# Kernel optimization log

Measured on AMD Instinct MI355X. Metric: run time of the kernel, lower is better.

The kernel has to match this reference:

```python
import jax, jax.numpy as jnp
import numpy as np

DIM = 256
HEADS = 8
HEAD_DIM = DIM // HEADS


def setup_inputs() -> dict:
    key = jax.random.key(0)
    ks = jax.random.split(key, 10)
    B, Nq, Nk, C = 2, 2048, 2048, DIM
    inp = {
        "query": jax.random.normal(ks[0], (B, Nq, C), jnp.float32),
        "key": jax.random.normal(ks[1], (B, Nk, C), jnp.float32),
        "value": jax.random.normal(ks[2], (B, Nk, C), jnp.float32),
        "qpos": jnp.zeros((B, Nq), jnp.int32),
        "kpos": jnp.zeros((B, Nk), jnp.int32),
        "mask": jax.random.randint(ks[3], (Nq, Nk), 0, 2) > 0,
        "similarities": jax.random.normal(ks[4], (B, HEADS, Nq, Nk), jnp.float32),
        # learned params (torch Linear stored here as [C_in, C_out]; no qkv bias)
        "Wq": jax.random.normal(ks[5], (C, C), jnp.float32) / np.sqrt(C),
        "Wk": jax.random.normal(ks[6], (C, C), jnp.float32) / np.sqrt(C),
        "Wv": jax.random.normal(ks[7], (C, C), jnp.float32) / np.sqrt(C),
        "Wp": jax.random.normal(ks[8], (C, C), jnp.float32) / np.sqrt(C),
        "bp": jax.random.normal(ks[9], (C,), jnp.float32) * 0.01,
    }
    return inp


def reference(query, key, value, qpos, kpos, mask, similarities, Wq, Wk, Wv, Wp, bp):
    B, Nq, C = query.shape
    Nk = key.shape[1]
    H, hd = HEADS, HEAD_DIM
    scale = hd ** -0.5
    # projections -> [B, N, H, hd] (rope is None, so qpos/kpos are unused)
    q = (query @ Wq).reshape(B, Nq, H, hd)
    k = (key @ Wk).reshape(B, Nk, H, hd)
    v = (value @ Wv).reshape(B, Nk, H, hd)
    # scores [B, H, Nq, Nk]
    attn = jnp.einsum("bqhd,bkhd->bhqk", q, k) * scale
    # mean-centered similarity bias (mean over heads, dim=1)
    attn = attn + (similarities - similarities.mean(axis=1, keepdims=True))
    # boolean mask: fill False positions with -inf, then softmax over keys
    attn = jnp.where(mask[None, None, :, :], attn, -jnp.inf)
    attn = jax.nn.softmax(attn, axis=-1)
    # AV -> [B, Nq, C], output projection
    x = jnp.einsum("bhqk,bkhd->bqhd", attn, v).reshape(B, Nq, C)
    return x @ Wp + bp
```

## Files before the change

### kernel.cpp

```cpp
#include <hip/hip_runtime.h>

#define B_  2
#define NQ  2048
#define NK  2048
#define C_  256
#define H_  8
#define HD  32

typedef float f32x4 __attribute__((ext_vector_type(4)));
typedef __bf16 bf16x8 __attribute__((ext_vector_type(8)));
typedef unsigned short ushort8 __attribute__((ext_vector_type(8)));

static __device__ __forceinline__ unsigned short f2bf(float f) {
    unsigned int u = __builtin_bit_cast(unsigned int, f);
    u += 0x7FFFu + ((u >> 16) & 1u);
    return (unsigned short)(u >> 16);
}
static __device__ __forceinline__ float bf2f(unsigned short h) {
    unsigned int u = ((unsigned int)h) << 16;
    return __builtin_bit_cast(float, u);
}
static __device__ __forceinline__ unsigned int split1(float f) {
    unsigned short h = f2bf(f);
    unsigned short l = f2bf(f - bf2f(h));
    return (unsigned int)h | ((unsigned int)l << 16);
}
static __device__ __forceinline__ bf16x8 ld_bf16x8(const unsigned short* p) {
    return __builtin_bit_cast(bf16x8, *(const ushort8*)p);
}
static __device__ __forceinline__ void async16(const void* g, void* l) {
    __builtin_amdgcn_global_load_lds((__attribute__((address_space(1))) void*)g,
                                     (__attribute__((address_space(3))) void*)l,
                                     16, 0, 0);
}

__global__ __launch_bounds__(256) void proj_kernel(const float* __restrict__ X,
                                                   const float* __restrict__ W,
                                                   unsigned short* __restrict__ dh,
                                                   unsigned short* __restrict__ dl,
                                                   int vmode)
{
    __shared__ unsigned short WtH[64][32];
    __shared__ unsigned short WtL[64][32];

    const int tid  = threadIdx.x;
    const int wave = tid >> 6;
    const int lane = tid & 63;
    const int n15  = lane & 15;
    const int quad = lane >> 4;
    const int m0   = blockIdx.x * 64;
    const int j0   = blockIdx.y * 64;

    f32x4 acc[4];
    acc[0] = 0.f; acc[1] = 0.f; acc[2] = 0.f; acc[3] = 0.f;

    const int sj  = tid >> 2;
    const int skc = (tid & 3) * 8;
    const float* __restrict__ xrow = X + (size_t)(m0 + wave * 16 + n15) * C_;

    for (int k0 = 0; k0 < C_; k0 += 32) {
        ushort8 wh, wl;
        #pragma unroll
        for (int i = 0; i < 8; ++i) {
            unsigned int p = split1(W[(size_t)(k0 + skc + i) * C_ + j0 + sj]);
            wh[i] = (unsigned short)p;
            wl[i] = (unsigned short)(p >> 16);
        }
        *(ushort8*)&WtH[sj][skc] = wh;
        *(ushort8*)&WtL[sj][skc] = wl;
        __syncthreads();

        f32x4 a0 = *(const f32x4*)(xrow + k0 + quad * 8);
        f32x4 a1 = *(const f32x4*)(xrow + k0 + quad * 8 + 4);
        ushort8 ah, al;
        #pragma unroll
        for (int i = 0; i < 4; ++i) {
            unsigned int p0 = split1(a0[i]);
            unsigned int p1 = split1(a1[i]);
            ah[i]     = (unsigned short)p0;  al[i]     = (unsigned short)(p0 >> 16);
            ah[i + 4] = (unsigned short)p1;  al[i + 4] = (unsigned short)(p1 >> 16);
        }
        bf16x8 Ah = __builtin_bit_cast(bf16x8, ah);
        bf16x8 Al = __builtin_bit_cast(bf16x8, al);

        #pragma unroll
        for (int f = 0; f < 4; ++f) {
            bf16x8 Bh = ld_bf16x8(&WtH[f * 16 + n15][quad * 8]);
            bf16x8 Bl = ld_bf16x8(&WtL[f * 16 + n15][quad * 8]);
            acc[f] = __builtin_amdgcn_mfma_f32_16x16x32_bf16(Al, Bl, acc[f], 0, 0, 0);
            acc[f] = __builtin_amdgcn_mfma_f32_16x16x32_bf16(Al, Bh, acc[f], 0, 0, 0);
            acc[f] = __builtin_amdgcn_mfma_f32_16x16x32_bf16(Ah, Bl, acc[f], 0, 0, 0);
            acc[f] = __builtin_amdgcn_mfma_f32_16x16x32_bf16(Ah, Bh, acc[f], 0, 0, 0);
        }
        __syncthreads();
    }

    #pragma unroll
    for (int f = 0; f < 4; ++f) {
        const int j = j0 + f * 16 + n15;
        const int h = j >> 5, dd = j & 31;
        #pragma unroll
        for (int r = 0; r < 4; ++r) {
            const int grow = m0 + wave * 16 + quad * 4 + r;
            const int b = grow >> 11, row = grow & 2047;
            unsigned int p = split1(acc[f][r]);
            size_t idx;
            if (vmode) idx = (size_t)((b * H_ + h) * HD + dd) * NK + row;
            else       idx = (size_t)((b * H_ + h) * NK + row) * HD + dd;
            dh[idx] = (unsigned short)p;
            dl[idx] = (unsigned short)(p >> 16);
        }
    }
}

__global__ __launch_bounds__(256) void outproj_kernel(const unsigned short* __restrict__ Xh,
                                                      const unsigned short* __restrict__ Xl,
                                                      const float* __restrict__ W,
                                                      const float* __restrict__ bias,
                                                      float* __restrict__ out)
{
    __shared__ unsigned short WtH[64][32];
    __shared__ unsigned short WtL[64][32];

    const int tid  = threadIdx.x;
    const int wave = tid >> 6;
    const int lane = tid & 63;
    const int n15  = lane & 15;
    const int quad = lane >> 4;
    const int m0   = blockIdx.x * 64;
    const int j0   = blockIdx.y * 64;

    f32x4 acc[4];
    acc[0] = 0.f; acc[1] = 0.f; acc[2] = 0.f; acc[3] = 0.f;

    const int sj  = tid >> 2;
    const int skc = (tid & 3) * 8;
    const size_t xoff = (size_t)(m0 + wave * 16 + n15) * C_;

    for (int k0 = 0; k0 < C_; k0 += 32) {
        ushort8 wh, wl;
        #pragma unroll
        for (int i = 0; i < 8; ++i) {
            unsigned int p = split1(W[(size_t)(k0 + skc + i) * C_ + j0 + sj]);
            wh[i] = (unsigned short)p;
            wl[i] = (unsigned short)(p >> 16);
        }
        *(ushort8*)&WtH[sj][skc] = wh;
        *(ushort8*)&WtL[sj][skc] = wl;
        __syncthreads();

        bf16x8 Ah = ld_bf16x8(Xh + xoff + k0 + quad * 8);
        bf16x8 Al = ld_bf16x8(Xl + xoff + k0 + quad * 8);

        #pragma unroll
        for (int f = 0; f < 4; ++f) {
            bf16x8 Bh = ld_bf16x8(&WtH[f * 16 + n15][quad * 8]);
            bf16x8 Bl = ld_bf16x8(&WtL[f * 16 + n15][quad * 8]);
            acc[f] = __builtin_amdgcn_mfma_f32_16x16x32_bf16(Al, Bl, acc[f], 0, 0, 0);
            acc[f] = __builtin_amdgcn_mfma_f32_16x16x32_bf16(Al, Bh, acc[f], 0, 0, 0);
            acc[f] = __builtin_amdgcn_mfma_f32_16x16x32_bf16(Ah, Bl, acc[f], 0, 0, 0);
            acc[f] = __builtin_amdgcn_mfma_f32_16x16x32_bf16(Ah, Bh, acc[f], 0, 0, 0);
        }
        __syncthreads();
    }

    #pragma unroll
    for (int f = 0; f < 4; ++f) {
        const int j = j0 + f * 16 + n15;
        const float bj = bias[j];
        #pragma unroll
        for (int r = 0; r < 4; ++r) {
            const int grow = m0 + wave * 16 + quad * 4 + r;
            out[(size_t)grow * C_ + j] = acc[f][r] + bj;
        }
    }
}

__global__ __launch_bounds__(512) void attn_kernel(const unsigned short* __restrict__ qh,
                                                   const unsigned short* __restrict__ ql,
                                                   const unsigned short* __restrict__ kh,
                                                   const unsigned short* __restrict__ kl,
                                                   const unsigned short* __restrict__ vh,
                                                   const unsigned short* __restrict__ vl,
                                                   const float* __restrict__ sim,
                                                   const int* __restrict__ mask,
                                                   unsigned short* __restrict__ xh,
                                                   unsigned short* __restrict__ xl)
{
    __shared__ float simLds[2][H_][16][32];
    __shared__ float biasLds[16][33];
    __shared__ float pLds[H_][16 * 32];

    const int tid  = threadIdx.x;
    const int wave = tid >> 6;
    const int lane = tid & 63;
    const int n15  = lane & 15;
    const int quad = lane >> 4;
    const int wg   = blockIdx.x;
    const int b    = wg >> 7;
    const int q0   = (wg & 127) * 16;

    const size_t bh   = (size_t)(b * H_ + wave);
    const size_t qoff = (bh * NQ + q0 + n15) * HD + quad * 8;
    const unsigned short* khb = kh + bh * NK * HD;
    const unsigned short* klb = kl + bh * NK * HD;
    const unsigned short* vhb = vh + bh * HD * NK;
    const unsigned short* vlb = vl + bh * HD * NK;
    const float* gsim = sim + (bh * NQ + q0) * (size_t)NK
                            + (size_t)(lane >> 3) * NK + (lane & 7) * 4;

    const bf16x8 Qh = ld_bf16x8(qh + qoff);
    const bf16x8 Ql = ld_bf16x8(ql + qoff);

    f32x4 O0 = 0.f, O1 = 0.f;
    float m_r[4] = {0.f, 0.f, 0.f, 0.f};
    float l_r[4] = {0.f, 0.f, 0.f, 0.f};

    async16(gsim,                  &simLds[0][wave][0][0]);
    async16(gsim + (size_t)8 * NK, &simLds[0][wave][8][0]);

    const float scale = 0.17677669529663687f;

    for (int it = 0; it < NK / 32; ++it) {
        const int k0  = it * 32;
        const int cur = it & 1;

        __syncthreads();

        {
            const int qq = tid >> 5, kk = tid & 31;
            float s = 0.f;
            #pragma unroll
            for (int h = 0; h < H_; ++h) s += simLds[cur][h][qq][kk];
            const int mk = mask[(size_t)(q0 + qq) * NK + k0 + kk];
            biasLds[qq][kk] = mk ? (-0.125f * s) : -1e30f;
        }
        __syncthreads();

        if (it + 1 < NK / 32) {
            const float* g = gsim + k0 + 32;
            async16(g,                  &simLds[cur ^ 1][wave][0][0]);
            async16(g + (size_t)8 * NK, &simLds[cur ^ 1][wave][8][0]);
        }

        const size_t koA = (size_t)(k0 + n15) * HD + quad * 8;
        const size_t koB = (size_t)(k0 + 16 + n15) * HD + quad * 8;
        bf16x8 Kh0 = ld_bf16x8(khb + koA), Kl0 = ld_bf16x8(klb + koA);
        bf16x8 Kh1 = ld_bf16x8(khb + koB), Kl1 = ld_bf16x8(klb + koB);

        f32x4 S0 = 0.f, S1 = 0.f;
        S0 = __builtin_amdgcn_mfma_f32_16x16x32_bf16(Ql, Kl0, S0, 0, 0, 0);
        S0 = __builtin_amdgcn_mfma_f32_16x16x32_bf16(Ql, Kh0, S0, 0, 0, 0);
        S0 = __builtin_amdgcn_mfma_f32_16x16x32_bf16(Qh, Kl0, S0, 0, 0, 0);
        S0 = __builtin_amdgcn_mfma_f32_16x16x32_bf16(Qh, Kh0, S0, 0, 0, 0);
        S1 = __builtin_amdgcn_mfma_f32_16x16x32_bf16(Ql, Kl1, S1, 0, 0, 0);
        S1 = __builtin_amdgcn_mfma_f32_16x16x32_bf16(Ql, Kh1, S1, 0, 0, 0);
        S1 = __builtin_amdgcn_mfma_f32_16x16x32_bf16(Qh, Kl1, S1, 0, 0, 0);
        S1 = __builtin_amdgcn_mfma_f32_16x16x32_bf16(Qh, Kh1, S1, 0, 0, 0);

        const size_t voA = (size_t)n15 * NK + k0 + quad * 8;
        const size_t voB = (size_t)(16 + n15) * NK + k0 + quad * 8;
        bf16x8 Vh0 = ld_bf16x8(vhb + voA), Vl0 = ld_bf16x8(vlb + voA);
        bf16x8 Vh1 = ld_bf16x8(vhb + voB), Vl1 = ld_bf16x8(vlb + voB);

        float P0[4], P1[4];
        #pragma unroll
        for (int r = 0; r < 4; ++r) {
            const int qq = quad * 4 + r;
            float s0 = S0[r] * scale + simLds[cur][wave][qq][n15]      + biasLds[qq][n15];
            float s1 = S1[r] * scale + simLds[cur][wave][qq][16 + n15] + biasLds[qq][16 + n15];

            float mx = fmaxf(s0, s1);
            #pragma unroll
            for (int off = 1; off < 16; off <<= 1) mx = fmaxf(mx, __shfl_xor(mx, off));
            const float mnew = fmaxf(m_r[r], mx);
            const float a  = __expf(m_r[r] - mnew);
            const float p0 = __expf(s0 - mnew);
            const float p1 = __expf(s1 - mnew);
            float sm = p0 + p1;
            #pragma unroll
            for (int off = 1; off < 16; off <<= 1) sm += __shfl_xor(sm, off);
            l_r[r] = l_r[r] * a + sm;
            m_r[r] = mnew;
            O0[r] *= a; O1[r] *= a;
            P0[r] = p0; P1[r] = p1;
        }

        float* pw = pLds[wave];
        #pragma unroll
        for (int r = 0; r < 4; ++r) {
            pw[(quad * 4 + r) * 32 + n15]      = P0[r];
            pw[(quad * 4 + r) * 32 + 16 + n15] = P1[r];
        }
        f32x4 pa = *(const f32x4*)(pw + n15 * 32 + quad * 8);
        f32x4 pb = *(const f32x4*)(pw + n15 * 32 + quad * 8 + 4);
        ushort8 phs, pls;
        #pragma unroll
        for (int i = 0; i < 4; ++i) {
            unsigned int pp0 = split1(pa[i]);
            unsigned int pp1 = split1(pb[i]);
            phs[i]     = (unsigned short)pp0;  pls[i]     = (unsigned short)(pp0 >> 16);
            phs[i + 4] = (unsigned short)pp1;  pls[i + 4] = (unsigned short)(pp1 >> 16);
        }
        bf16x8 Ph = __builtin_bit_cast(bf16x8, phs);
        bf16x8 Pl = __builtin_bit_cast(bf16x8, pls);

        O0 = __builtin_amdgcn_mfma_f32_16x16x32_bf16(Pl, Vl0, O0, 0, 0, 0);
        O0 = __builtin_amdgcn_mfma_f32_16x16x32_bf16(Pl, Vh0, O0, 0, 0, 0);
        O0 = __builtin_amdgcn_mfma_f32_16x16x32_bf16(Ph, Vl0, O0, 0, 0, 0);
        O0 = __builtin_amdgcn_mfma_f32_16x16x32_bf16(Ph, Vh0, O0, 0, 0, 0);
        O1 = __builtin_amdgcn_mfma_f32_16x16x32_bf16(Pl, Vl1, O1, 0, 0, 0);
        O1 = __builtin_amdgcn_mfma_f32_16x16x32_bf16(Pl, Vh1, O1, 0, 0, 0);
        O1 = __builtin_amdgcn_mfma_f32_16x16x32_bf16(Ph, Vl1, O1, 0, 0, 0);
        O1 = __builtin_amdgcn_mfma_f32_16x16x32_bf16(Ph, Vh1, O1, 0, 0, 0);
    }

    #pragma unroll
    for (int r = 0; r < 4; ++r) {
        const int q = q0 + quad * 4 + r;
        const float inv = 1.0f / l_r[r];
        const size_t base = (size_t)(b * NQ + q) * C_ + wave * HD;
        unsigned int p0 = split1(O0[r] * inv);
        unsigned int p1 = split1(O1[r] * inv);
        xh[base + n15]      = (unsigned short)p0;
        xl[base + n15]      = (unsigned short)(p0 >> 16);
        xh[base + 16 + n15] = (unsigned short)p1;
        xl[base + 16 + n15] = (unsigned short)(p1 >> 16);
    }
}

extern "C" void kernel_launch(void* const* d_in, const int* in_sizes, int n_in,
                              void* d_out, int out_size, void* d_ws, size_t ws_size,
                              hipStream_t stream) {
    const float* query = (const float*)d_in[0];
    const float* key   = (const float*)d_in[1];
    const float* value = (const float*)d_in[2];
    const int*   mask  = (const int*)d_in[5];
    const float* sim   = (const float*)d_in[6];
    const float* Wq  = (const float*)d_in[7];
    const float* Wk  = (const float*)d_in[8];
    const float* Wv  = (const float*)d_in[9];
    const float* Wp  = (const float*)d_in[10];
    const float* bp  = (const float*)d_in[11];
    float* out = (float*)d_out;

    const size_t NEL = (size_t)B_ * H_ * NQ * HD;
    unsigned short* qbh = (unsigned short*)d_ws;
    unsigned short* qbl = qbh + NEL;
    unsigned short* kbh = qbl + NEL;
    unsigned short* kbl = kbh + NEL;
    unsigned short* vbh = kbl + NEL;
    unsigned short* vbl = vbh + NEL;
    unsigned short* xbh = vbl + NEL;
    unsigned short* xbl = xbh + NEL;

    dim3 g(64, 4, 1);
    proj_kernel<<<g, 256, 0, stream>>>(query, Wq, qbh, qbl, 0);
    proj_kernel<<<g, 256, 0, stream>>>(key,   Wk, kbh, kbl, 0);
    proj_kernel<<<g, 256, 0, stream>>>(value, Wv, vbh, vbl, 1);
    attn_kernel<<<256, 512, 0, stream>>>(qbh, qbl, kbh, kbl, vbh, vbl, sim, mask, xbh, xbl);
    outproj_kernel<<<g, 256, 0, stream>>>(xbh, xbl, Wp, bp, out);
}
```

Baseline: 610.7 us.

## Split attention over key segments with combine pass, fuse QKV projections

Splits each attention workgroup's key range into four segments so the grid grows from 256 to 1024 workgroups. The per-segment partial outputs, row maxima and row sums go to a workspace, and a new combine kernel merges them with log-sum-exp rescaling. The change also merges the three projection launches into one grid with a z dimension, prefetches the mask asynchronously into LDS, and stores P to LDS as bf16 hi/lo halves instead of fp32. The intent is to fill the GPU's compute units and hide latency, at the cost of an extra kernel launch and partial-result traffic.

After: 568.5 us. -6.9%, faster.

```diff
diff --git a/kernel.cpp b/kernel.cpp
--- a/kernel.cpp
+++ b/kernel.cpp
@@ -6,6 +6,11 @@
 #define C_  256
 #define H_  8
 #define HD  32
+#define SPLIT 4
+#define KSEG (NK / SPLIT)
+#define KT   (KSEG / 32)
+#define QT_  (NQ / 16)
+#define PART_STRIDE 544
 
 typedef float f32x4 __attribute__((ext_vector_type(4)));
 typedef __bf16 bf16x8 __attribute__((ext_vector_type(8)));
@@ -34,14 +39,24 @@
                                      16, 0, 0);
 }
 
-__global__ __launch_bounds__(256) void proj_kernel(const float* __restrict__ X,
-                                                   const float* __restrict__ W,
-                                                   unsigned short* __restrict__ dh,
-                                                   unsigned short* __restrict__ dl,
-                                                   int vmode)
+__global__ __launch_bounds__(256) void proj_kernel(
+        const float* __restrict__ query, const float* __restrict__ key,
+        const float* __restrict__ value,
+        const float* __restrict__ Wq, const float* __restrict__ Wk,
+        const float* __restrict__ Wv,
+        unsigned short* __restrict__ qbh, unsigned short* __restrict__ qbl,
+        unsigned short* __restrict__ kbh, unsigned short* __restrict__ kbl,
+        unsigned short* __restrict__ vbh, unsigned short* __restrict__ vbl)
 {
     __shared__ unsigned short WtH[64][32];
     __shared__ unsigned short WtL[64][32];
+
+    const int z = blockIdx.z;
+    const float* X = (z == 0) ? query : (z == 1) ? key : value;
+    const float* W = (z == 0) ? Wq    : (z == 1) ? Wk  : Wv;
+    unsigned short* dh = (z == 0) ? qbh : (z == 1) ? kbh : vbh;
+    unsigned short* dl = (z == 0) ? qbl : (z == 1) ? kbl : vbl;
+    const int vmode = (z == 2);
 
     const int tid  = threadIdx.x;
     const int wave = tid >> 6;
@@ -176,29 +191,31 @@
     }
 }
 
-__global__ __launch_bounds__(512) void attn_kernel(const unsigned short* __restrict__ qh,
-                                                   const unsigned short* __restrict__ ql,
-                                                   const unsigned short* __restrict__ kh,
-                                                   const unsigned short* __restrict__ kl,
-                                                   const unsigned short* __restrict__ vh,
-                                                   const unsigned short* __restrict__ vl,
-                                                   const float* __restrict__ sim,
-                                                   const int* __restrict__ mask,
-                                                   unsigned short* __restrict__ xh,
-                                                   unsigned short* __restrict__ xl)
+__global__ __launch_bounds__(512, 6) void attn_kernel(
+        const unsigned short* __restrict__ qh, const unsigned short* __restrict__ ql,
+        const unsigned short* __restrict__ kh, const unsigned short* __restrict__ kl,
+        const unsigned short* __restrict__ vh, const unsigned short* __restrict__ vl,
+        const float* __restrict__ sim, const int* __restrict__ mask,
+        float* __restrict__ part)
 {
     __shared__ float simLds[2][H_][16][32];
+    __shared__ int   maskLds[2][16][32];
     __shared__ float biasLds[16][33];
-    __shared__ float pLds[H_][16 * 32];
+    __shared__ __align__(16) unsigned short pLds[H_][16 * 40];
 
     const int tid  = threadIdx.x;
     const int wave = tid >> 6;
     const int lane = tid & 63;
     const int n15  = lane & 15;
     const int quad = lane >> 4;
+
     const int wg   = blockIdx.x;
-    const int b    = wg >> 7;
-    const int q0   = (wg & 127) * 16;
+    const int s    = wg >> 8;
+    const int rem  = wg & 255;
+    const int b    = rem >> 7;
+    const int qt   = rem & 127;
+    const int q0   = qt * 16;
+    const int kbeg = s * KSEG;
 
     const size_t bh   = (size_t)(b * H_ + wave);
     const size_t qoff = (bh * NQ + q0 + n15) * HD + quad * 8;
@@ -206,8 +223,9 @@
     const unsigned short* klb = kl + bh * NK * HD;
     const unsigned short* vhb = vh + bh * HD * NK;
     const unsigned short* vlb = vl + bh * HD * NK;
-    const float* gsim = sim + (bh * NQ + q0) * (size_t)NK
+    const float* gsim = sim + (bh * NQ + q0) * (size_t)NK + kbeg
                             + (size_t)(lane >> 3) * NK + (lane & 7) * 4;
+    const int* gmask = mask + (size_t)(q0 + (lane >> 3)) * NK + kbeg + (lane & 7) * 4;
 
     const bf16x8 Qh = ld_bf16x8(qh + qoff);
     const bf16x8 Ql = ld_bf16x8(ql + qoff);
@@ -218,29 +236,37 @@
 
     async16(gsim,                  &simLds[0][wave][0][0]);
     async16(gsim + (size_t)8 * NK, &simLds[0][wave][8][0]);
+    if (wave == 0) {
+        async16(gmask,                  &maskLds[0][0][0]);
+        async16(gmask + (size_t)8 * NK, &maskLds[0][8][0]);
+    }
 
     const float scale = 0.17677669529663687f;
 
-    for (int it = 0; it < NK / 32; ++it) {
-        const int k0  = it * 32;
+    for (int it = 0; it < KT; ++it) {
+        const int k0  = kbeg + it * 32;
         const int cur = it & 1;
 
         __syncthreads();
 
         {
             const int qq = tid >> 5, kk = tid & 31;
-            float s = 0.f;
+            float sum = 0.f;
             #pragma unroll
-            for (int h = 0; h < H_; ++h) s += simLds[cur][h][qq][kk];
-            const int mk = mask[(size_t)(q0 + qq) * NK + k0 + kk];
-            biasLds[qq][kk] = mk ? (-0.125f * s) : -1e30f;
-        }
-        __syncthreads();
-
-        if (it + 1 < NK / 32) {
-            const float* g = gsim + k0 + 32;
+            for (int h = 0; h < H_; ++h) sum += simLds[cur][h][qq][kk];
+            biasLds[qq][kk] = maskLds[cur][qq][kk] ? (-0.125f * sum) : -1e30f;
+        }
+        __syncthreads();
+
+        if (it + 1 < KT) {
+            const float* g  = gsim + it * 32 + 32;
             async16(g,                  &simLds[cur ^ 1][wave][0][0]);
             async16(g + (size_t)8 * NK, &simLds[cur ^ 1][wave][8][0]);
+            if (wave == 0) {
+                const int* gm = gmask + it * 32 + 32;
+                async16(gm,                  &maskLds[cur ^ 1][0][0]);
+                async16(gm + (size_t)8 * NK, &maskLds[cur ^ 1][8][0]);
+            }
         }
 
         const size_t koA = (size_t)(k0 + n15) * HD + quad * 8;
@@ -263,7 +289,7 @@
         bf16x8 Vh0 = ld_bf16x8(vhb + voA), Vl0 = ld_bf16x8(vlb + voA);
         bf16x8 Vh1 = ld_bf16x8(vhb + voB), Vl1 = ld_bf16x8(vlb + voB);
 
-        float P0[4], P1[4];
+        unsigned int u0[4], u1[4];
         #pragma unroll
         for (int r = 0; r < 4; ++r) {
             const int qq = quad * 4 + r;
@@ -283,27 +309,24 @@
             l_r[r] = l_r[r] * a + sm;
             m_r[r] = mnew;
             O0[r] *= a; O1[r] *= a;
-            P0[r] = p0; P1[r] = p1;
-        }
-
-        float* pw = pLds[wave];
+            u0[r] = split1(p0); u1[r] = split1(p1);
+        }
+
+        unsigned short* pw = pLds[wave];
         #pragma unroll
         for (int r = 0; r < 4; ++r) {
-            pw[(quad * 4 + r) * 32 + n15]      = P0[r];
-            pw[(quad * 4 + r) * 32 + 16 + n15] = P1[r];
-        }
-        f32x4 pa = *(const f32x4*)(pw + n15 * 32 + quad * 8);
-        f32x4 pb = *(const f32x4*)(pw + n15 * 32 + quad * 8 + 4);
-        ushort8 phs, pls;
-        #pragma unroll
-        for (int i = 0; i < 4; ++i) {
-            unsigned int pp0 = split1(pa[i]);
-            unsigned int pp1 = split1(pb[i]);
-            phs[i]     = (unsigned short)pp0;  pls[i]     = (unsigned short)(pp0 >> 16);
-            phs[i + 4] = (unsigned short)pp1;  pls[i + 4] = (unsigned short)(pp1 >> 16);
-        }
-        bf16x8 Ph = __builtin_bit_cast(bf16x8, phs);
-        bf16x8 Pl = __builtin_bit_cast(bf16x8, pls);
+            const int qq = quad * 4 + r;
+            pw[qq * 40 + n15]      = (unsigned short)u0[r];
+            pw[qq * 40 + 16 + n15] = (unsigned short)u1[r];
+        }
+        bf16x8 Ph = ld_bf16x8(pw + n15 * 40 + quad * 8);
+        #pragma unroll
+        for (int r = 0; r < 4; ++r) {
+            const int qq = quad * 4 + r;
+            pw[qq * 40 + n15]      = (unsigned short)(u0[r] >> 16);
+            pw[qq * 40 + 16 + n15] = (unsigned short)(u1[r] >> 16);
+        }
+        bf16x8 Pl = ld_bf16x8(pw + n15 * 40 + quad * 8);
 
         O0 = __builtin_amdgcn_mfma_f32_16x16x32_bf16(Pl, Vl0, O0, 0, 0, 0);
         O0 = __builtin_amdgcn_mfma_f32_16x16x32_bf16(Pl, Vh0, O0, 0, 0, 0);
@@ -315,17 +338,62 @@
         O1 = __builtin_amdgcn_mfma_f32_16x16x32_bf16(Ph, Vh1, O1, 0, 0, 0);
     }
 
+    float* pb = part + (size_t)(((s * B_ + b) * H_ + wave) * QT_ + qt) * PART_STRIDE;
     #pragma unroll
     for (int r = 0; r < 4; ++r) {
-        const int q = q0 + quad * 4 + r;
-        const float inv = 1.0f / l_r[r];
-        const size_t base = (size_t)(b * NQ + q) * C_ + wave * HD;
-        unsigned int p0 = split1(O0[r] * inv);
-        unsigned int p1 = split1(O1[r] * inv);
-        xh[base + n15]      = (unsigned short)p0;
-        xl[base + n15]      = (unsigned short)(p0 >> 16);
-        xh[base + 16 + n15] = (unsigned short)p1;
-        xl[base + 16 + n15] = (unsigned short)(p1 >> 16);
+        const int q = quad * 4 + r;
+        pb[q * 32 + n15]      = O0[r];
+        pb[q * 32 + 16 + n15] = O1[r];
+        if (n15 == 0) {
+            pb[512 + q] = m_r[r];
+            pb[528 + q] = l_r[r];
+        }
+    }
+}
+
+__global__ __launch_bounds__(256) void combine_kernel(const float* __restrict__ part,
+                                                      unsigned short* __restrict__ xh,
+                                                      unsigned short* __restrict__ xl)
+{
+    const int wid  = blockIdx.x * 4 + (threadIdx.x >> 6);
+    const int lane = threadIdx.x & 63;
+    const int b  = wid >> 10;
+    const int h  = (wid >> 7) & 7;
+    const int qt = wid & 127;
+    const int q  = lane >> 2;
+    const int d0 = (lane & 3) * 8;
+
+    float ms[SPLIT], ls[SPLIT];
+    float mstar = -1e30f;
+    #pragma unroll
+    for (int s = 0; s < SPLIT; ++s) {
+        const float* pb = part + (size_t)(((s * B_ + b) * H_ + h) * QT_ + qt) * PART_STRIDE;
+        ms[s] = pb[512 + q];
+        ls[s] = pb[528 + q];
+        mstar = fmaxf(mstar, ms[s]);
+    }
+    f32x4 acc0 = 0.f, acc1 = 0.f;
+    float lsum = 0.f;
+    #pragma unroll
+    for (int s = 0; s < SPLIT; ++s) {
+        const float* pb = part + (size_t)(((s * B_ + b) * H_ + h) * QT_ + qt) * PART_STRIDE;
+        const float w = __expf(ms[s] - mstar);
+        lsum += w * ls[s];
+        f32x4 o0 = *(const f32x4*)(pb + q * 32 + d0);
+        f32x4 o1 = *(const f32x4*)(pb + q * 32 + d0 + 4);
+        acc0 += w * o0;
+        acc1 += w * o1;
+    }
+    const float inv = 1.0f / lsum;
+    const size_t base = (size_t)(b * NQ + qt * 16 + q) * C_ + h * HD + d0;
+    #pragma unroll
+    for (int i = 0; i < 4; ++i) {
+        unsigned int p0 = split1(acc0[i] * inv);
+        unsigned int p1 = split1(acc1[i] * inv);
+        xh[base + i]     = (unsigned short)p0;
+        xl[base + i]     = (unsigned short)(p0 >> 16);
+        xh[base + 4 + i] = (unsigned short)p1;
+        xl[base + 4 + i] = (unsigned short)(p1 >> 16);
     }
 }
 
@@ -353,11 +421,12 @@
     unsigned short* vbl = vbh + NEL;
     unsigned short* xbh = vbl + NEL;
     unsigned short* xbl = xbh + NEL;
-
-    dim3 g(64, 4, 1);
-    proj_kernel<<<g, 256, 0, stream>>>(query, Wq, qbh, qbl, 0);
-    proj_kernel<<<g, 256, 0, stream>>>(key,   Wk, kbh, kbl, 0);
-    proj_kernel<<<g, 256, 0, stream>>>(value, Wv, vbh, vbl, 1);
-    attn_kernel<<<256, 512, 0, stream>>>(qbh, qbl, kbh, kbl, vbh, vbl, sim, mask, xbh, xbl);
-    outproj_kernel<<<g, 256, 0, stream>>>(xbh, xbl, Wp, bp, out);
-}
+    float* part = (float*)(xbl + NEL);
+
+    proj_kernel<<<dim3(64, 4, 3), 256, 0, stream>>>(query, key, value, Wq, Wk, Wv,
+                                                    qbh, qbl, kbh, kbl, vbh, vbl);
+    attn_kernel<<<SPLIT * 256, 512, 0, stream>>>(qbh, qbl, kbh, kbl, vbh, vbl,
+                                                 sim, mask, part);
+    combine_kernel<<<512, 256, 0, stream>>>(part, xbh, xbl);
+    outproj_kernel<<<dim3(64, 4), 256, 0, stream>>>(xbh, xbl, Wp, bp, out);
+}
```
